# Performance work log

Measured on AMD Instinct MI355X. Metric: run time of the kernel, lower is better.

## Reference

```python
import jax, jax.numpy as jnp
import numpy as np

B, S, D = 8, 2048, 768

def setup_inputs() -> dict:
    key = jax.random.key(0)
    k1, k2, k3, k4 = jax.random.split(key, 4)
    scale = 1.0 / np.sqrt(D)
    x = jax.random.normal(k1, (B, S, D), dtype=jnp.float32)
    W = jax.random.normal(k2, (D, D), dtype=jnp.float32) * scale
    proj_w = jax.random.normal(k3, (D, D), dtype=jnp.float32) * scale
    proj_b = jax.random.normal(k4, (D,), dtype=jnp.float32) * scale
    return {"x": x, "W": W, "proj_w": proj_w, "proj_b": proj_b}


def reference(x, W, proj_w, proj_b):
    # Wx = Linear(x) with torch convention: x @ W.T  -> [B,S,D]
    Wx = jnp.einsum('bsd,ed->bse', x, W)
    # s = Wx @ x^T  -> [B,S,S]
    s = jnp.einsum('bse,bte->bst', Wx, x)
    # mask diagonal (self) with -inf
    eye = jnp.eye(S, dtype=bool)
    s = jnp.where(eye[None, :, :], -jnp.inf, s)
    a = jax.nn.softmax(s, axis=2)
    # c = a @ x -> [B,S,D]
    c = jnp.einsum('bst,btd->bsd', a, x)
    # proj + relu, residual; dropout with p=0 is identity
    c = jax.nn.relu(jnp.einsum('bsd,ed->bse', c, proj_w) + proj_b)
    return x + c
```

## Files before the change

kernel.cpp:

```cpp
#include <hip/hip_runtime.h>
#include <hip/hip_bf16.h>

typedef _Float16 fp16_t;
typedef __attribute__((ext_vector_type(8))) _Float16 fp16x8;
typedef __attribute__((ext_vector_type(4))) _Float16 fp16x4;
typedef __attribute__((ext_vector_type(4))) float fx4;

#define GLDS(g, l)                                                              \
  __builtin_amdgcn_global_load_lds(                                             \
      (const __attribute__((address_space(1))) void*)(g),                       \
      (__attribute__((address_space(3))) void*)(l), 16, 0, 0)

enum { EPI_F32 = 0, EPI_F16 = 1, EPI_FUSE = 2, EPI_SOFT = 3 };

__device__ __forceinline__ void xcd_decode(int& bx, int& by, int& bz) {
  const int nx = gridDim.x, ny = gridDim.y;
  const int lid = (int)(blockIdx.x + nx * (blockIdx.y + ny * blockIdx.z));
  const int j = lid & 7, k = lid >> 3;
  bx = k % nx;
  const int s = j + 8 * (k / nx);
  by = s % ny;
  bz = s / ny;
}

template <bool ASPLIT, int EPI>
__global__ __launch_bounds__(256) void gemm_bt(
    const fp16_t* __restrict__ A1, const fp16_t* __restrict__ A2,
    const fp16_t* __restrict__ B1, void* __restrict__ Cv, int K, int lda,
    int ldb, long long sA, long long sB, long long sC,
    const float* __restrict__ bias, const float* __restrict__ resid,
    float* __restrict__ m_out, float* __restrict__ l_out) {
  constexpr int ALO = ASPLIT ? 128 * 32 : 0;
  __shared__ __align__(16) fp16_t As[2][128 * 32 + ALO];
  __shared__ __align__(16) fp16_t Bs[2][128 * 32];
  __shared__ float smax[(EPI == EPI_SOFT) ? 256 : 1];
  __shared__ float ssum[(EPI == EPI_SOFT) ? 256 : 1];

  const int tid  = threadIdx.x;
  const int lane = tid & 63;
  const int w    = tid >> 6;
  const int wr   = w >> 1;
  const int wc   = w & 1;

  int bx, by, bz;
  xcd_decode(bx, by, bz);
  const int N = (int)gridDim.x * 128;
  const long long tile_m = (long long)by * 128;
  const long long tile_n = (long long)bx * 128;
  const long long z = bz;
  const long long aoff = z * sA + tile_m * (long long)lda;
  const long long boff = z * sB + tile_n * (long long)ldb;

  fx4 acc[4][4];
#pragma unroll
  for (int i = 0; i < 4; i++)
#pragma unroll
    for (int j = 0; j < 4; j++) acc[i][j] = (fx4){0.f, 0.f, 0.f, 0.f};

  const int r_l = lane >> 2;
  const int c_l = ((((lane & 3) + ((r_l >> 1) & 3)) & 3) << 3);
  const int frow = lane & 15;
  const int qoff = (((lane >> 4) - ((frow >> 1) & 3)) & 3) << 3;

  const size_t sa0 = (size_t)(w * 16 + r_l) * lda + c_l;
  const size_t sa1 = (size_t)(64 + w * 16 + r_l) * lda + c_l;
  const size_t sb0 = (size_t)(w * 16 + r_l) * ldb + c_l;
  const size_t sb1 = (size_t)(64 + w * 16 + r_l) * ldb + c_l;
  const int ld0 = (w * 16) * 32;
  const int ld1 = (64 + w * 16) * 32;

  for (int kt = 0; kt < K; kt += 64) {
    __syncthreads();
#pragma unroll
    for (int h = 0; h < 2; h++) {
      const fp16_t* gah = A1 + aoff + kt + h * 32;
      const fp16_t* gbh = B1 + boff + kt + h * 32;
      GLDS(gah + sa0, &As[h][ld0]);
      GLDS(gah + sa1, &As[h][ld1]);
      GLDS(gbh + sb0, &Bs[h][ld0]);
      GLDS(gbh + sb1, &Bs[h][ld1]);
      if (ASPLIT) {
        const fp16_t* gal = A2 + aoff + kt + h * 32;
        GLDS(gal + sa0, &As[h][ALO + ld0]);
        GLDS(gal + sa1, &As[h][ALO + ld1]);
      }
    }
    __syncthreads();

#pragma unroll
    for (int h = 0; h < 2; h++) {
      fp16x8 afh[4], bbh[4], afl[4];
#pragma unroll
      for (int mi = 0; mi < 4; mi++)
        afh[mi] = *(const fp16x8*)&As[h][(wr * 64 + mi * 16 + frow) * 32 + qoff];
#pragma unroll
      for (int ni = 0; ni < 4; ni++)
        bbh[ni] = *(const fp16x8*)&Bs[h][(wc * 64 + ni * 16 + frow) * 32 + qoff];
      if (ASPLIT) {
#pragma unroll
        for (int mi = 0; mi < 4; mi++)
          afl[mi] =
              *(const fp16x8*)&As[h][ALO + (wr * 64 + mi * 16 + frow) * 32 + qoff];
      }
#pragma unroll
      for (int mi = 0; mi < 4; mi++)
#pragma unroll
        for (int ni = 0; ni < 4; ni++) {
          fx4 a = acc[mi][ni];
          a = __builtin_amdgcn_mfma_f32_16x16x32_f16(afh[mi], bbh[ni], a, 0, 0, 0);
          if (ASPLIT)
            a = __builtin_amdgcn_mfma_f32_16x16x32_f16(afl[mi], bbh[ni], a, 0, 0, 0);
          acc[mi][ni] = a;
        }
    }
  }

  const int er = (lane >> 4) * 4;
  const int ec = lane & 15;
  const long long crow = tile_m + wr * 64;
  const long long ccol = tile_n + wc * 64;

  if constexpr (EPI == EPI_SOFT) {
#pragma unroll
    for (int mi = 0; mi < 4; mi++)
#pragma unroll
      for (int j = 0; j < 4; j++) {
        const long long r = crow + mi * 16 + er + j;
        float mx = -1e30f;
#pragma unroll
        for (int ni = 0; ni < 4; ni++) {
          const long long cc = ccol + ni * 16 + ec;
          float v = acc[mi][ni][j];
          if (r == cc) v = -1e30f;
          acc[mi][ni][j] = v;
          mx = fmaxf(mx, v);
        }
#pragma unroll
        for (int o = 1; o < 16; o <<= 1) mx = fmaxf(mx, __shfl_xor(mx, o, 64));
        if (ec == 0) smax[wc * 128 + wr * 64 + mi * 16 + er + j] = mx;
      }
    __syncthreads();
#pragma unroll
    for (int mi = 0; mi < 4; mi++)
#pragma unroll
      for (int j = 0; j < 4; j++) {
        const int rid = wr * 64 + mi * 16 + er + j;
        const float m = fmaxf(smax[rid], smax[128 + rid]);
        const long long r = crow + mi * 16 + er + j;
        float s = 0.f;
#pragma unroll
        for (int ni = 0; ni < 4; ni++) {
          const float e = __expf(acc[mi][ni][j] - m);
          s += e;
          ((fp16_t*)Cv)[z * sC + r * N + (ccol + ni * 16 + ec)] = (fp16_t)e;
        }
#pragma unroll
        for (int o = 1; o < 16; o <<= 1) s += __shfl_xor(s, o, 64);
        if (ec == 0) ssum[wc * 128 + rid] = s;
      }
    __syncthreads();
    if (tid < 128) {
      const long long si = (z * 16 + bx) * 2048 + tile_m + tid;
      m_out[si] = fmaxf(smax[tid], smax[128 + tid]);
      l_out[si] = ssum[tid] + ssum[128 + tid];
    }
  } else {
#pragma unroll
    for (int mi = 0; mi < 4; mi++)
#pragma unroll
      for (int j = 0; j < 4; j++) {
        const long long r = crow + mi * 16 + er + j;
#pragma unroll
        for (int ni = 0; ni < 4; ni++) {
          const long long cc = ccol + ni * 16 + ec;
          const long long idx = z * sC + r * N + cc;
          const float v = acc[mi][ni][j];
          if (EPI == EPI_F32) {
            ((float*)Cv)[idx] = v;
          } else if (EPI == EPI_F16) {
            ((fp16_t*)Cv)[idx] = (fp16_t)v;
          } else {
            float u = v + bias[cc];
            u = u > 0.f ? u : 0.f;
            ((float*)Cv)[idx] = resid[r * N + cc] + u;
          }
        }
      }
  }
}

__global__ __launch_bounds__(256) void gemm_pv(
    const fp16_t* __restrict__ P, const float* __restrict__ mstat,
    const float* __restrict__ lstat, const fp16_t* __restrict__ Bx,
    fp16_t* __restrict__ C) {
  __shared__ __align__(16) fp16_t As[2][128 * 32];
  __shared__ __align__(16) fp16_t Bs[2][128 * 32];
  __shared__ float sc[16][128];

  const int tid  = threadIdx.x;
  const int lane = tid & 63;
  const int w    = tid >> 6;
  const int wr   = w >> 1;
  const int wc   = w & 1;

  int bx, by, bz;
  xcd_decode(bx, by, bz);
  const long long tile_m = (long long)by * 128;
  const long long tile_n = (long long)bx * 128;
  const long long z = bz;

  if (tid < 128) {
    const long long base = z * 16 * 2048 + tile_m + tid;
    float mv[16];
    float m = -1e30f;
#pragma unroll
    for (int t = 0; t < 16; t++) {
      mv[t] = mstat[base + t * 2048];
      m = fmaxf(m, mv[t]);
    }
    float l = 0.f;
#pragma unroll
    for (int t = 0; t < 16; t++) l += lstat[base + t * 2048] * __expf(mv[t] - m);
    const float il = 1.0f / l;
#pragma unroll
    for (int t = 0; t < 16; t++) sc[t][tid] = __expf(mv[t] - m) * il;
  }

  fx4 acc[4][4];
#pragma unroll
  for (int i = 0; i < 4; i++)
#pragma unroll
    for (int j = 0; j < 4; j++) acc[i][j] = (fx4){0.f, 0.f, 0.f, 0.f};

  const int r_l = lane >> 2;
  const int c_l = ((((lane & 3) + ((r_l >> 1) & 3)) & 3) << 3);
  const int frow = lane & 15;
  const int qoff = (((lane >> 4) - ((frow >> 1) & 3)) & 3) << 3;
  const size_t s0 = (size_t)(w * 16 + r_l) * 2048 + c_l;
  const size_t s1 = (size_t)(64 + w * 16 + r_l) * 2048 + c_l;
  const int ld0 = (w * 16) * 32;
  const int ld1 = (64 + w * 16) * 32;

  const fp16_t* A = P + z * (2048LL * 2048) + tile_m * 2048;
  const fp16_t* B = Bx + z * (768LL * 2048) + tile_n * 2048;

  for (int kt = 0; kt < 2048; kt += 64) {
    __syncthreads();
#pragma unroll
    for (int h = 0; h < 2; h++) {
      GLDS(A + kt + h * 32 + s0, &As[h][ld0]);
      GLDS(A + kt + h * 32 + s1, &As[h][ld1]);
      GLDS(B + kt + h * 32 + s0, &Bs[h][ld0]);
      GLDS(B + kt + h * 32 + s1, &Bs[h][ld1]);
    }
    __syncthreads();

    fp16_t sh[4];
    {
      const int tt = kt >> 7;
#pragma unroll
      for (int mi = 0; mi < 4; mi++)
        sh[mi] = (fp16_t)sc[tt][wr * 64 + mi * 16 + frow];
    }

#pragma unroll
    for (int h = 0; h < 2; h++) {
      fp16x8 af[4], bb[4];
#pragma unroll
      for (int mi = 0; mi < 4; mi++) {
        af[mi] = *(const fp16x8*)&As[h][(wr * 64 + mi * 16 + frow) * 32 + qoff];
        af[mi] *= sh[mi];
      }
#pragma unroll
      for (int ni = 0; ni < 4; ni++)
        bb[ni] = *(const fp16x8*)&Bs[h][(wc * 64 + ni * 16 + frow) * 32 + qoff];
#pragma unroll
      for (int mi = 0; mi < 4; mi++)
#pragma unroll
        for (int ni = 0; ni < 4; ni++)
          acc[mi][ni] = __builtin_amdgcn_mfma_f32_16x16x32_f16(
              af[mi], bb[ni], acc[mi][ni], 0, 0, 0);
    }
  }

  const int er = (lane >> 4) * 4;
  const int ec = lane & 15;
  const long long crow = tile_m + wr * 64;
  const long long ccol = tile_n + wc * 64;
  fp16_t* Cz = C + z * (2048LL * 768);
#pragma unroll
  for (int mi = 0; mi < 4; mi++)
#pragma unroll
    for (int j = 0; j < 4; j++) {
      const long long rr = crow + mi * 16 + er + j;
#pragma unroll
      for (int ni = 0; ni < 4; ni++)
        Cz[rr * 768 + ccol + ni * 16 + ec] = (fp16_t)acc[mi][ni][j];
    }
}

__global__ __launch_bounds__(256) void prep_x(
    const float* __restrict__ x, fp16_t* __restrict__ xh,
    fp16_t* __restrict__ xl, fp16_t* __restrict__ xT) {
  __shared__ fp16_t t[32][33];
  const int b = blockIdx.z;
  const int d0 = blockIdx.x * 32;
  const int s0 = blockIdx.y * 32;
  const float* ib = x + (long long)b * 2048 * 768;
  const int tx = threadIdx.x & 31;
  const int ty = threadIdx.x >> 5;
#pragma unroll
  for (int i = 0; i < 4; i++) {
    const int srow = s0 + ty + i * 8;
    const long long idx = (long long)b * 2048 * 768 + (long long)srow * 768 + d0 + tx;
    const float v = ib[(long long)srow * 768 + d0 + tx];
    const fp16_t h = (fp16_t)v;
    xh[idx] = h;
    xl[idx] = (fp16_t)(v - (float)h);
    t[ty + i * 8][tx] = h;
  }
  __syncthreads();
#pragma unroll
  for (int i = 0; i < 4; i++)
    xT[(long long)b * 768 * 2048 + (long long)(d0 + ty + i * 8) * 2048 + s0 + tx] =
        t[tx][ty + i * 8];
}

__global__ __launch_bounds__(256) void cast2_f32_f16(
    const float* __restrict__ a, const float* __restrict__ b,
    fp16_t* __restrict__ oa, fp16_t* __restrict__ ob, int n4) {
  const int i = blockIdx.x * 256 + threadIdx.x;
  if (i >= n4) return;
  const float* in = blockIdx.y == 0 ? a : b;
  fp16_t* out = blockIdx.y == 0 ? oa : ob;
  const float4 v = ((const float4*)in)[i];
  ((fp16x4*)out)[i] =
      (fp16x4){(fp16_t)v.x, (fp16_t)v.y, (fp16_t)v.z, (fp16_t)v.w};
}

extern "C" void kernel_launch(void* const* d_in, const int* in_sizes, int n_in,
                              void* d_out, int out_size, void* d_ws,
                              size_t ws_size, hipStream_t stream) {
  const float* x  = (const float*)d_in[0];
  const float* W  = (const float*)d_in[1];
  const float* pw = (const float*)d_in[2];
  const float* pb = (const float*)d_in[3];

  const long long S = 2048, D = 768;
  const long long BS = 8 * S;

  char* p = (char*)d_ws;
  auto carve = [&](long long bytes) {
    char* q = p;
    p += (bytes + 255) & ~255LL;
    return q;
  };
  fp16_t* xh = (fp16_t*)carve(BS * D * 2);
  fp16_t* xl = (fp16_t*)carve(BS * D * 2);
  fp16_t* xT = (fp16_t*)carve(BS * D * 2);
  fp16_t* Wx = (fp16_t*)carve(BS * D * 2);
  fp16_t* Wh = (fp16_t*)carve(D * D * 2);
  fp16_t* ph = (fp16_t*)carve(D * D * 2);
  float*  mstat = (float*)carve(BS * 16 * 4);
  float*  lstat = (float*)carve(BS * 16 * 4);
  fp16_t* Ps = (fp16_t*)carve(8 * S * S * 2);
  fp16_t* cb = Wx;

  prep_x<<<dim3(24, 64, 8), 256, 0, stream>>>(x, xh, xl, xT);
  cast2_f32_f16<<<dim3((unsigned)(D * D / 4 / 256), 2), 256, 0, stream>>>(
      W, pw, Wh, ph, (int)(D * D / 4));

  gemm_bt<true, EPI_F16><<<dim3(6, 128, 1), 256, 0, stream>>>(
      xh, xl, Wh, Wx, 768, 768, 768, 0, 0, 0, nullptr, nullptr, nullptr,
      nullptr);

  gemm_bt<false, EPI_SOFT><<<dim3(16, 16, 8), 256, 0, stream>>>(
      Wx, nullptr, xh, Ps, 768, 768, 768, S * D, S * D, S * S, nullptr,
      nullptr, mstat, lstat);

  gemm_pv<<<dim3(6, 16, 8), 256, 0, stream>>>(Ps, mstat, lstat, xT, cb);

  gemm_bt<false, EPI_FUSE><<<dim3(6, 128, 1), 256, 0, stream>>>(
      cb, nullptr, ph, (float*)d_out, 768, 768, 768, 0, 0, 0, pb, x, nullptr,
      nullptr);
}
```

Measured before the change: 364.7 us.

## Double-buffer K-halves with async LDS loads overlapping MFMA compute

Restructures the GEMM main loops of both kernels so the two 32-wide K halves act as a ping-pong buffer. The next half's global_load_lds is issued before computing on the current half, with explicit vmcnt waits and sched-barrier-wrapped s_barriers replacing the two __syncthreads per iteration. This is meant to hide global-to-LDS latency behind the MFMA work. It relies on hand-counted vmcnt values and scheduler fences, which are fragile if the compiler emits other vector memory ops. A __syncthreads is added after the softmax scale setup so the sc table is visible before use.

```diff
diff --git a/kernel.cpp b/kernel.cpp
--- a/kernel.cpp
+++ b/kernel.cpp
@@ -10,6 +10,13 @@
   __builtin_amdgcn_global_load_lds(                                             \
       (const __attribute__((address_space(1))) void*)(g),                       \
       (__attribute__((address_space(3))) void*)(l), 16, 0, 0)
+
+#define PBAR()                                                                  \
+  do {                                                                          \
+    __builtin_amdgcn_sched_barrier(0);                                          \
+    __builtin_amdgcn_s_barrier();                                               \
+    __builtin_amdgcn_sched_barrier(0);                                          \
+  } while (0)
 
 enum { EPI_F32 = 0, EPI_F16 = 1, EPI_FUSE = 2, EPI_SOFT = 3 };
 
@@ -69,50 +76,63 @@
   const int ld0 = (w * 16) * 32;
   const int ld1 = (64 + w * 16) * 32;
 
+  auto stage = [&](int b, int kk) {
+    const fp16_t* gah = A1 + aoff + kk;
+    const fp16_t* gbh = B1 + boff + kk;
+    GLDS(gah + sa0, &As[b][ld0]);
+    GLDS(gah + sa1, &As[b][ld1]);
+    GLDS(gbh + sb0, &Bs[b][ld0]);
+    GLDS(gbh + sb1, &Bs[b][ld1]);
+    if (ASPLIT) {
+      const fp16_t* gal = A2 + aoff + kk;
+      GLDS(gal + sa0, &As[b][ALO + ld0]);
+      GLDS(gal + sa1, &As[b][ALO + ld1]);
+    }
+  };
+  auto compute = [&](int b) {
+    fp16x8 afh[4], bbh[4], afl[4];
+#pragma unroll
+    for (int mi = 0; mi < 4; mi++)
+      afh[mi] = *(const fp16x8*)&As[b][(wr * 64 + mi * 16 + frow) * 32 + qoff];
+#pragma unroll
+    for (int ni = 0; ni < 4; ni++)
+      bbh[ni] = *(const fp16x8*)&Bs[b][(wc * 64 + ni * 16 + frow) * 32 + qoff];
+    if (ASPLIT) {
+#pragma unroll
+      for (int mi = 0; mi < 4; mi++)
+        afl[mi] =
+            *(const fp16x8*)&As[b][ALO + (wr * 64 + mi * 16 + frow) * 32 + qoff];
+    }
+#pragma unroll
+    for (int mi = 0; mi < 4; mi++)
+#pragma unroll
+      for (int ni = 0; ni < 4; ni++) {
+        fx4 a = acc[mi][ni];
+        a = __builtin_amdgcn_mfma_f32_16x16x32_f16(afh[mi], bbh[ni], a, 0, 0, 0);
+        if (ASPLIT)
+          a = __builtin_amdgcn_mfma_f32_16x16x32_f16(afl[mi], bbh[ni], a, 0, 0, 0);
+        acc[mi][ni] = a;
+      }
+  };
+
+  stage(0, 0);
   for (int kt = 0; kt < K; kt += 64) {
-    __syncthreads();
-#pragma unroll
-    for (int h = 0; h < 2; h++) {
-      const fp16_t* gah = A1 + aoff + kt + h * 32;
-      const fp16_t* gbh = B1 + boff + kt + h * 32;
-      GLDS(gah + sa0, &As[h][ld0]);
-      GLDS(gah + sa1, &As[h][ld1]);
-      GLDS(gbh + sb0, &Bs[h][ld0]);
-      GLDS(gbh + sb1, &Bs[h][ld1]);
-      if (ASPLIT) {
-        const fp16_t* gal = A2 + aoff + kt + h * 32;
-        GLDS(gal + sa0, &As[h][ALO + ld0]);
-        GLDS(gal + sa1, &As[h][ALO + ld1]);
-      }
-    }
-    __syncthreads();
-
-#pragma unroll
-    for (int h = 0; h < 2; h++) {
-      fp16x8 afh[4], bbh[4], afl[4];
-#pragma unroll
-      for (int mi = 0; mi < 4; mi++)
-        afh[mi] = *(const fp16x8*)&As[h][(wr * 64 + mi * 16 + frow) * 32 + qoff];
-#pragma unroll
-      for (int ni = 0; ni < 4; ni++)
-        bbh[ni] = *(const fp16x8*)&Bs[h][(wc * 64 + ni * 16 + frow) * 32 + qoff];
-      if (ASPLIT) {
-#pragma unroll
-        for (int mi = 0; mi < 4; mi++)
-          afl[mi] =
-              *(const fp16x8*)&As[h][ALO + (wr * 64 + mi * 16 + frow) * 32 + qoff];
-      }
-#pragma unroll
-      for (int mi = 0; mi < 4; mi++)
-#pragma unroll
-        for (int ni = 0; ni < 4; ni++) {
-          fx4 a = acc[mi][ni];
-          a = __builtin_amdgcn_mfma_f32_16x16x32_f16(afh[mi], bbh[ni], a, 0, 0, 0);
-          if (ASPLIT)
-            a = __builtin_amdgcn_mfma_f32_16x16x32_f16(afl[mi], bbh[ni], a, 0, 0, 0);
-          acc[mi][ni] = a;
-        }
-    }
+    stage(1, kt + 32);
+    if (ASPLIT) asm volatile("s_waitcnt vmcnt(6)" ::: "memory");
+    else        asm volatile("s_waitcnt vmcnt(4)" ::: "memory");
+    PBAR();
+    compute(0);
+    PBAR();
+    if (kt + 64 < K) {
+      stage(0, kt + 64);
+      if (ASPLIT) asm volatile("s_waitcnt vmcnt(6)" ::: "memory");
+      else        asm volatile("s_waitcnt vmcnt(4)" ::: "memory");
+    } else {
+      asm volatile("s_waitcnt vmcnt(0)" ::: "memory");
+    }
+    PBAR();
+    compute(1);
+    PBAR();
   }
 
   const int er = (lane >> 4) * 4;
@@ -225,6 +245,7 @@
 #pragma unroll
     for (int t = 0; t < 16; t++) sc[t][tid] = __expf(mv[t] - m) * il;
   }
+  __syncthreads();
 
   fx4 acc[4][4];
 #pragma unroll
@@ -244,17 +265,32 @@
   const fp16_t* A = P + z * (2048LL * 2048) + tile_m * 2048;
   const fp16_t* B = Bx + z * (768LL * 2048) + tile_n * 2048;
 
+  auto stage = [&](int b, int kk) {
+    GLDS(A + kk + s0, &As[b][ld0]);
+    GLDS(A + kk + s1, &As[b][ld1]);
+    GLDS(B + kk + s0, &Bs[b][ld0]);
+    GLDS(B + kk + s1, &Bs[b][ld1]);
+  };
+  auto compute = [&](int b, const fp16_t* sh) {
+    fp16x8 af[4], bb[4];
+#pragma unroll
+    for (int mi = 0; mi < 4; mi++) {
+      af[mi] = *(const fp16x8*)&As[b][(wr * 64 + mi * 16 + frow) * 32 + qoff];
+      af[mi] *= sh[mi];
+    }
+#pragma unroll
+    for (int ni = 0; ni < 4; ni++)
+      bb[ni] = *(const fp16x8*)&Bs[b][(wc * 64 + ni * 16 + frow) * 32 + qoff];
+#pragma unroll
+    for (int mi = 0; mi < 4; mi++)
+#pragma unroll
+      for (int ni = 0; ni < 4; ni++)
+        acc[mi][ni] = __builtin_amdgcn_mfma_f32_16x16x32_f16(
+            af[mi], bb[ni], acc[mi][ni], 0, 0, 0);
+  };
+
+  stage(0, 0);
   for (int kt = 0; kt < 2048; kt += 64) {
-    __syncthreads();
-#pragma unroll
-    for (int h = 0; h < 2; h++) {
-      GLDS(A + kt + h * 32 + s0, &As[h][ld0]);
-      GLDS(A + kt + h * 32 + s1, &As[h][ld1]);
-      GLDS(B + kt + h * 32 + s0, &Bs[h][ld0]);
-      GLDS(B + kt + h * 32 + s1, &Bs[h][ld1]);
-    }
-    __syncthreads();
-
     fp16_t sh[4];
     {
       const int tt = kt >> 7;
@@ -262,25 +298,20 @@
       for (int mi = 0; mi < 4; mi++)
         sh[mi] = (fp16_t)sc[tt][wr * 64 + mi * 16 + frow];
     }
-
-#pragma unroll
-    for (int h = 0; h < 2; h++) {
-      fp16x8 af[4], bb[4];
-#pragma unroll
-      for (int mi = 0; mi < 4; mi++) {
-        af[mi] = *(const fp16x8*)&As[h][(wr * 64 + mi * 16 + frow) * 32 + qoff];
-        af[mi] *= sh[mi];
-      }
-#pragma unroll
-      for (int ni = 0; ni < 4; ni++)
-        bb[ni] = *(const fp16x8*)&Bs[h][(wc * 64 + ni * 16 + frow) * 32 + qoff];
-#pragma unroll
-      for (int mi = 0; mi < 4; mi++)
-#pragma unroll
-        for (int ni = 0; ni < 4; ni++)
-          acc[mi][ni] = __builtin_amdgcn_mfma_f32_16x16x32_f16(
-              af[mi], bb[ni], acc[mi][ni], 0, 0, 0);
-    }
+    stage(1, kt + 32);
+    asm volatile("s_waitcnt vmcnt(4)" ::: "memory");
+    PBAR();
+    compute(0, sh);
+    PBAR();
+    if (kt + 64 < 2048) {
+      stage(0, kt + 64);
+      asm volatile("s_waitcnt vmcnt(4)" ::: "memory");
+    } else {
+      asm volatile("s_waitcnt vmcnt(0)" ::: "memory");
+    }
+    PBAR();
+    compute(1, sh);
+    PBAR();
   }
 
   const int er = (lane >> 4) * 4;
```

Measured after the change: 367.2 us. About the same (+0.7%).
